# Optimization experiments

Hardware: AMD Instinct MI355X
Metric: run time of the kernel (lower is better)

## Reference

```python
import jax, jax.numpy as jnp
import numpy as np

NUM_HEADS = 16
ROTARY_BASE = 10000.0


def _rope_cos_sin(seqlen, rotary_dim, dtype):
    # inv_freq: (rotary_dim/2,), cos/sin: (seqlen, rotary_dim/2)
    inv_freq = 1.0 / (ROTARY_BASE ** (jnp.arange(0, rotary_dim, 2, dtype=jnp.float32) / rotary_dim))
    t = jnp.arange(seqlen, dtype=jnp.float32)
    freqs = jnp.outer(t, inv_freq)
    return jnp.cos(freqs).astype(dtype), jnp.sin(freqs).astype(dtype)


def _apply_rotary(x, cos, sin):
    # x: (b, s, h, d); cos/sin: (s, d/2). Non-interleaved (GPT-NeoX) halves.
    d2 = cos.shape[-1]
    x1, x2 = x[..., :d2], x[..., d2:2 * d2]
    c = cos[None, :, None, :]
    s = sin[None, :, None, :]
    r1 = x1 * c - x2 * s
    r2 = x1 * s + x2 * c
    return jnp.concatenate([r1, r2], axis=-1)


def setup_inputs() -> dict:
    key = jax.random.key(0)
    ks = jax.random.split(key, 5)
    B, S, E = 2, 2048, 2048
    x = jax.random.normal(ks[0], (B, S, E), dtype=jnp.float32)
    wqkv_w = jax.random.normal(ks[1], (3 * E, E), dtype=jnp.float32) * 0.02
    wqkv_b = jax.random.normal(ks[2], (3 * E,), dtype=jnp.float32) * 0.02
    out_w = jax.random.normal(ks[3], (E, E), dtype=jnp.float32) * 0.02
    out_b = jax.random.normal(ks[4], (E,), dtype=jnp.float32) * 0.02
    return {"x": x, "wqkv_w": wqkv_w, "wqkv_b": wqkv_b, "out_w": out_w, "out_b": out_b}


def reference(x, wqkv_w, wqkv_b, out_w, out_b):
    B, S, E = x.shape
    H = NUM_HEADS
    D = E // H
    # fused QKV projection: (b, s, 3, h, d)
    qkv = (jnp.einsum('bse,fe->bsf', x, wqkv_w) + wqkv_b).reshape(B, S, 3, H, D)
    q, k, v = qkv[:, :, 0], qkv[:, :, 1], qkv[:, :, 2]
    # rotary embedding on full head_dim of q and k
    cos, sin = _rope_cos_sin(S, D, x.dtype)
    q = _apply_rotary(q, cos, sin)
    k = _apply_rotary(k, cos, sin)
    # causal self-attention, softmax_scale = 1/sqrt(head_dim)
    scale = 1.0 / jnp.sqrt(jnp.asarray(D, dtype=x.dtype))
    scores = jnp.einsum('bshd,bthd->bhst', q, k) * scale
    causal_mask = jnp.tril(jnp.ones((S, S), dtype=bool))
    scores = jnp.where(causal_mask[None, None], scores, jnp.asarray(-1e30, dtype=scores.dtype))
    attn = jax.nn.softmax(scores, axis=-1)
    ctx = jnp.einsum('bhst,bthd->bshd', attn, v).reshape(B, S, E)
    return jnp.einsum('bse,fe->bsf', ctx, out_w) + out_b
```

## Files before the change

kernel.cpp:

```cpp
#include <hip/hip_runtime.h>

typedef unsigned short u16;
typedef unsigned int u32;
typedef __bf16 bf16x8 __attribute__((ext_vector_type(8)));
typedef float fx4 __attribute__((ext_vector_type(4)));

__device__ __forceinline__ float bf2f(u16 u) {
    return __uint_as_float(((u32)u) << 16);
}
__device__ __forceinline__ u16 f2bf(float f) {
    u32 x = __float_as_uint(f);
    u32 r = (x + 0x7fffu + ((x >> 16) & 1u)) >> 16;
    return (u16)r;
}

__device__ __forceinline__ void gld16(const u16* g, u16* l) {
    __builtin_amdgcn_global_load_lds(
        (const __attribute__((address_space(1))) void*)g,
        (__attribute__((address_space(3))) void*)l, 16, 0, 0);
}

#define MFMA16(a, b, c) __builtin_amdgcn_mfma_f32_16x16x32_bf16((a), (b), (c), 0, 0, 0)

__global__ __launch_bounds__(256) void cvt_kernel(const float* __restrict__ x,
                                                  const float* __restrict__ w1,
                                                  const float* __restrict__ w2,
                                                  u16* __restrict__ xb,
                                                  u16* __restrict__ w1b,
                                                  u16* __restrict__ w2b) {
    size_t g = ((size_t)blockIdx.x * 256 + threadIdx.x) * 8;
    const float* src;
    u16* dst;
    if (g < 8388608) {
        src = x;
        dst = xb;
    } else if (g < 20971520) {
        src = w1 - 8388608;
        dst = w1b - 8388608;
    } else {
        src = w2 - 20971520;
        dst = w2b - 20971520;
    }
    float4 a = *(const float4*)&src[g];
    float4 b = *(const float4*)&src[g + 4];
    u16 v[8];
    v[0] = f2bf(a.x);
    v[1] = f2bf(a.y);
    v[2] = f2bf(a.z);
    v[3] = f2bf(a.w);
    v[4] = f2bf(b.x);
    v[5] = f2bf(b.y);
    v[6] = f2bf(b.z);
    v[7] = f2bf(b.w);
    *(uint4*)&dst[g] = *(const uint4*)v;
}

template <int MODE>
__global__ __launch_bounds__(256, 2) void gemm_bt(const u16* __restrict__ A,
                                                  const u16* __restrict__ B,
                                                  const float* __restrict__ bias,
                                                  float* __restrict__ Cf,
                                                  u16* __restrict__ qb,
                                                  u16* __restrict__ kb,
                                                  u16* __restrict__ vb,
                                                  int N, int K) {
    __shared__ __align__(16) u16 As[2][128 * 32];
    __shared__ __align__(16) u16 Bs[2][128 * 32];

    const int tid = threadIdx.x;
    const int lane = tid & 63;
    const int wave = tid >> 6;
    const int quad = lane >> 4;
    const int m16 = lane & 15;
    const int wm = wave >> 1, wn = wave & 1;
    const int bm = blockIdx.y * 128, bn = blockIdx.x * 128;

    const int r0 = tid >> 2;
    const int u0 = (tid & 3) ^ ((r0 >> 1) & 3);
    const int r1 = (tid + 256) >> 2;
    const int u1 = ((tid + 256) & 3) ^ ((r1 >> 1) & 3);
    const u16* a0 = &A[(size_t)(bm + r0) * K + u0 * 8];
    const u16* a1 = &A[(size_t)(bm + r1) * K + u1 * 8];
    const u16* b0 = &B[(size_t)(bn + r0) * K + u0 * 8];
    const u16* b1 = &B[(size_t)(bn + r1) * K + u1 * 8];

    const int su = (quad ^ ((m16 >> 1) & 3)) * 8;

#define GLDT(kt_, buf_)                                                       \
    {                                                                         \
        const int k0_ = (kt_) << 5;                                           \
        gld16(a0 + k0_, &As[buf_][tid * 8]);                                  \
        gld16(a1 + k0_, &As[buf_][(tid + 256) * 8]);                          \
        gld16(b0 + k0_, &Bs[buf_][tid * 8]);                                  \
        gld16(b1 + k0_, &Bs[buf_][(tid + 256) * 8]);                          \
    }

    const fx4 zero4 = {0.f, 0.f, 0.f, 0.f};
    fx4 acc[4][4];
#pragma unroll
    for (int i = 0; i < 4; ++i)
#pragma unroll
        for (int j = 0; j < 4; ++j) acc[i][j] = zero4;

    const int nk = K >> 5;
    GLDT(0, 0);
    if (nk > 1) {
        GLDT(1, 1);
        asm volatile("s_waitcnt vmcnt(4)" ::: "memory");
    } else {
        asm volatile("s_waitcnt vmcnt(0)" ::: "memory");
    }
    __builtin_amdgcn_s_barrier();

    int cur = 0;
    for (int kt = 0; kt < nk; ++kt) {
        bf16x8 af[4], bfr[4];
#pragma unroll
        for (int t = 0; t < 4; ++t) {
            af[t] = *(const bf16x8*)&As[cur][(wm * 64 + t * 16 + m16) * 32 + su];
            bfr[t] = *(const bf16x8*)&Bs[cur][(wn * 64 + t * 16 + m16) * 32 + su];
        }
        __builtin_amdgcn_s_setprio(1);
#pragma unroll
        for (int mt = 0; mt < 4; ++mt)
#pragma unroll
            for (int nt = 0; nt < 4; ++nt)
                acc[mt][nt] = MFMA16(af[mt], bfr[nt], acc[mt][nt]);
        __builtin_amdgcn_s_setprio(0);
        __builtin_amdgcn_sched_barrier(0);
        asm volatile("s_waitcnt lgkmcnt(0)" ::: "memory");
        __builtin_amdgcn_s_barrier();

        if (kt + 2 < nk) {
            GLDT(kt + 2, cur);
            asm volatile("s_waitcnt vmcnt(4)" ::: "memory");
        } else {
            asm volatile("s_waitcnt vmcnt(0)" ::: "memory");
        }
        __builtin_amdgcn_s_barrier();
        cur ^= 1;
    }

#pragma unroll
    for (int mt = 0; mt < 4; ++mt) {
#pragma unroll
        for (int r = 0; r < 4; ++r) {
            int row = bm + wm * 64 + mt * 16 + quad * 4 + r;
#pragma unroll
            for (int nt = 0; nt < 4; ++nt) {
                int col = bn + wn * 64 + nt * 16 + m16;
                float v = acc[mt][nt][r] + bias[col];
                if (MODE == 0) {
                    Cf[(size_t)row * N + col] = v;
                } else {
                    int which = col >> 11;
                    int h = (col >> 7) & 15;
                    int d = col & 127;
                    int b = row >> 11;
                    int s = row & 2047;
                    u16* dst = (which == 0) ? qb : ((which == 1) ? kb : vb);
                    dst[(size_t)((b * 16 + h) * 2048 + s) * 128 + d] = f2bf(v);
                }
            }
        }
    }
#undef GLDT
}

__global__ __launch_bounds__(256) void rope_kernel(u16* __restrict__ q,
                                                   u16* __restrict__ k) {
    int t = blockIdx.x * 256 + threadIdx.x;
    int i = t & 63;
    int s = (t >> 6) & 2047;
    int bh = t >> 17;
    float inv = exp2f(-(float)i * 0.2076205059304595f);
    float ang = (float)s * inv;
    float sn, cs;
    sincosf(ang, &sn, &cs);
    size_t base = ((size_t)bh * 2048 + s) * 128 + i;
    {
        float x1 = bf2f(q[base]), x2 = bf2f(q[base + 64]);
        q[base] = f2bf(x1 * cs - x2 * sn);
        q[base + 64] = f2bf(x1 * sn + x2 * cs);
    }
    {
        float x1 = bf2f(k[base]), x2 = bf2f(k[base + 64]);
        k[base] = f2bf(x1 * cs - x2 * sn);
        k[base + 64] = f2bf(x1 * sn + x2 * cs);
    }
}

__global__ __launch_bounds__(256) void vtrans_kernel(const u16* __restrict__ v,
                                                     u16* __restrict__ vt) {
    __shared__ __align__(16) u16 L[128 * 66];
    const int tid = threadIdx.x;
    const int kb = blockIdx.x * 64;
    const int bh = blockIdx.y;
    const u16* vp = v + (size_t)bh * 2048 * 128;
    u16* op = vt + (size_t)bh * 128 * 2048;
#pragma unroll
    for (int i = 0; i < 4; ++i) {
        int c = i * 256 + tid;
        int t = c >> 4, d8 = (c & 15) << 3;
        uint4 x = *(const uint4*)&vp[(kb + t) * 128 + d8];
        const u16* xs = (const u16*)&x;
#pragma unroll
        for (int j = 0; j < 8; ++j) L[(d8 + j) * 66 + t] = xs[j];
    }
    __syncthreads();
#pragma unroll
    for (int i = 0; i < 4; ++i) {
        int c = i * 256 + tid;
        int d = c >> 3, t8 = (c & 7) << 3;
        uint4 x;
        u16* xs = (u16*)&x;
#pragma unroll
        for (int j = 0; j < 8; ++j) xs[j] = L[d * 66 + t8 + j];
        *(uint4*)&op[(size_t)d * 2048 + kb + t8] = x;
    }
}

__global__ __launch_bounds__(512, 2) void attn_kernel(const u16* __restrict__ q,
                                                      const u16* __restrict__ k,
                                                      const u16* __restrict__ vt,
                                                      u16* __restrict__ ctx) {
    __shared__ __align__(16) u16 Ks[2][64 * 128];
    __shared__ __align__(16) u16 Vs[2][128 * 64];
    __shared__ __align__(16) u16 Ps[8][16 * 64];

    const int tid = threadIdx.x;
    const int lane = tid & 63;
    const int wave = tid >> 6;
    const int quad = lane >> 4;
    const int m16 = lane & 15;

    const int l = blockIdx.x;
    const int qt0 = l & 7;
    const int bh = l >> 3;
    const int b = bh >> 4, h = bh & 15;
    const u16* qp = q + (size_t)bh * 2048 * 128;
    const u16* kp = k + (size_t)bh * 2048 * 128;
    const u16* vp = vt + (size_t)bh * 128 * 2048;
    const float scale = 0.08838834764831845f;
    const fx4 zero4 = {0.f, 0.f, 0.f, 0.f};

    int ksrc[2], vsrc[2];
#pragma unroll
    for (int i = 0; i < 2; ++i) {
        int s = tid + i * 512;
        int r = s >> 4, p = s & 15;
        ksrc[i] = r * 128 + (p ^ (r & 7)) * 8;
        int d = s >> 3, pv = s & 7;
        vsrc[i] = d * 2048 + (pv ^ (d & 7)) * 8;
    }

#define GLD_TILE(kb_, buf_)                                                   \
    {                                                                         \
        _Pragma("unroll") for (int ii = 0; ii < 2; ++ii) {                    \
            gld16(kp + (size_t)(kb_)*128 + ksrc[ii],                          \
                  &Ks[buf_][tid * 8 + ii * 4096]);                            \
            gld16(vp + (kb_) + vsrc[ii], &Vs[buf_][tid * 8 + ii * 4096]);     \
        }                                                                     \
    }

#pragma unroll 1
    for (int pass = 0; pass < 2; ++pass) {
        const int qt = pass ? (15 - qt0) : qt0;
        const int qrow0 = qt * 128 + wave * 16;
        const int nkt = 2 * qt + 2;

        bf16x8 qf[4];
#pragma unroll
        for (int c = 0; c < 4; ++c)
            qf[c] = *(const bf16x8*)&qp[(size_t)(qrow0 + m16) * 128 + c * 32 +
                                        quad * 8];

        fx4 o[8];
#pragma unroll
        for (int dn = 0; dn < 8; ++dn) o[dn] = zero4;
        float mi[4], li[4];
#pragma unroll
        for (int r = 0; r < 4; ++r) {
            mi[r] = -1e30f;
            li[r] = 0.f;
        }

        GLD_TILE(0, 0);
        __syncthreads();
        int cur = 0;
        for (int kt = 0; kt < nkt; ++kt) {
            const int kb = kt * 64;
            if (kt + 1 < nkt) GLD_TILE(kb + 64, cur ^ 1);

            fx4 sc[4];
#pragma unroll
            for (int nt = 0; nt < 4; ++nt) sc[nt] = zero4;
            __builtin_amdgcn_s_setprio(1);
#pragma unroll
            for (int c = 0; c < 4; ++c)
#pragma unroll
                for (int nt = 0; nt < 4; ++nt) {
                    int e = (nt * 16 + m16) * 128 + c * 32 + quad * 8;
                    bf16x8 kf =
                        *(const bf16x8*)&Ks[cur][e ^ ((m16 & 7) << 3)];
                    sc[nt] = MFMA16(qf[c], kf, sc[nt]);
                }
            __builtin_amdgcn_s_setprio(0);

#pragma unroll
            for (int r = 0; r < 4; ++r) {
                int rg = qrow0 + quad * 4 + r;
                float mx = mi[r];
#pragma unroll
                for (int nt = 0; nt < 4; ++nt) {
                    int cg = kb + nt * 16 + m16;
                    float s = sc[nt][r] * scale;
                    s = (cg <= rg) ? s : -1e30f;
                    sc[nt][r] = s;
                    mx = fmaxf(mx, s);
                }
                mx = fmaxf(mx, __shfl_xor(mx, 1));
                mx = fmaxf(mx, __shfl_xor(mx, 2));
                mx = fmaxf(mx, __shfl_xor(mx, 4));
                mx = fmaxf(mx, __shfl_xor(mx, 8));
                float alpha = __expf(mi[r] - mx);
                mi[r] = mx;
                float rsum = 0.f;
                int row = quad * 4 + r;
#pragma unroll
                for (int nt = 0; nt < 4; ++nt) {
                    float p = __expf(sc[nt][r] - mx);
                    Ps[wave][(row * 64 + nt * 16 + m16) ^ ((row & 7) << 3)] =
                        f2bf(p);
                    rsum += p;
                }
                rsum += __shfl_xor(rsum, 1);
                rsum += __shfl_xor(rsum, 2);
                rsum += __shfl_xor(rsum, 4);
                rsum += __shfl_xor(rsum, 8);
                li[r] = li[r] * alpha + rsum;
#pragma unroll
                for (int dn = 0; dn < 8; ++dn) o[dn][r] *= alpha;
            }

            __builtin_amdgcn_s_setprio(1);
#pragma unroll
            for (int c2 = 0; c2 < 2; ++c2) {
                bf16x8 pf = *(const bf16x8*)&Ps[wave][(m16 * 64 + c2 * 32 +
                                                       quad * 8) ^
                                                      ((m16 & 7) << 3)];
#pragma unroll
                for (int dn = 0; dn < 8; ++dn) {
                    int e = (dn * 16 + m16) * 64 + c2 * 32 + quad * 8;
                    bf16x8 vf =
                        *(const bf16x8*)&Vs[cur][e ^ ((m16 & 7) << 3)];
                    o[dn] = MFMA16(pf, vf, o[dn]);
                }
            }
            __builtin_amdgcn_s_setprio(0);

            __syncthreads();
            cur ^= 1;
        }

#pragma unroll
        for (int r = 0; r < 4; ++r) {
            int row = qrow0 + quad * 4 + r;
            float inv = 1.0f / li[r];
#pragma unroll
            for (int dn = 0; dn < 8; ++dn) {
                int d = dn * 16 + m16;
                ctx[((size_t)(b * 2048 + row)) * 2048 + h * 128 + d] =
                    f2bf(o[dn][r] * inv);
            }
        }
    }
}

extern "C" void kernel_launch(void* const* d_in, const int* in_sizes, int n_in,
                              void* d_out, int out_size, void* d_ws,
                              size_t ws_size, hipStream_t stream) {
    const float* x = (const float*)d_in[0];
    const float* wqkv_w = (const float*)d_in[1];
    const float* wqkv_b = (const float*)d_in[2];
    const float* out_w = (const float*)d_in[3];
    const float* out_b = (const float*)d_in[4];
    u16* ws = (u16*)d_ws;

    u16* xb = ws;
    u16* wqkvb = ws + 8388608;
    u16* vb = ws + 20971520;
    u16* outwb = ws + 29360128;
    u16* vtb = xb;
    u16* ctx = vb;
    u16* qb = (u16*)d_out;
    u16* kb = qb + 8388608;

    cvt_kernel<<<12288, 256, 0, stream>>>(x, wqkv_w, out_w, xb, wqkvb, outwb);
    gemm_bt<1><<<dim3(48, 32), 256, 0, stream>>>(xb, wqkvb, wqkv_b, nullptr,
                                                 qb, kb, vb, 6144, 2048);
    rope_kernel<<<16384, 256, 0, stream>>>(qb, kb);
    vtrans_kernel<<<dim3(32, 32), 256, 0, stream>>>(vb, vtb);
    attn_kernel<<<256, 512, 0, stream>>>(qb, kb, vtb, ctx);
    gemm_bt<0><<<dim3(16, 32), 256, 0, stream>>>(ctx, outwb, out_b,
                                                 (float*)d_out, nullptr,
                                                 nullptr, nullptr, 2048, 2048);
}
```

Before: 418.2 us.

## Add dedicated 256x128-tile QKV GEMM kernel with 8 waves and split-K phases

Replaces the generic 128x128 gemm_bt instantiation for the QKV projection with a specialized kernel using 512 threads and a 256x128 output tile. It loads 64-wide K slabs as two 32-wide halves into double-buffered LDS and interleaves each prefetch with MFMA work, using explicit waitcnt and priority hints. The aim is more reuse of each B tile across rows and better latency hiding, at the cost of more LDS per block and possibly lower occupancy. The epilogue still scatters bias-added bf16 results into per-head Q/K/V layouts.

```diff
diff --git a/kernel.cpp b/kernel.cpp
--- a/kernel.cpp
+++ b/kernel.cpp
@@ -55,6 +55,111 @@
     *(uint4*)&dst[g] = *(const uint4*)v;
 }
 
+__global__ __launch_bounds__(512, 2) void gemm_qkv(const u16* __restrict__ A,
+                                                   const u16* __restrict__ B,
+                                                   const float* __restrict__ bias,
+                                                   u16* __restrict__ qb,
+                                                   u16* __restrict__ kb,
+                                                   u16* __restrict__ vb) {
+    const int K = 2048;
+    __shared__ __align__(16) u16 As[2][2][256 * 32];
+    __shared__ __align__(16) u16 Bs[2][2][128 * 32];
+
+    const int tid = threadIdx.x;
+    const int lane = tid & 63;
+    const int wave = tid >> 6;
+    const int quad = lane >> 4;
+    const int m16 = lane & 15;
+    const int wm = wave >> 1;
+    const int wn = wave & 1;
+
+    const int bm = (blockIdx.x / 48) * 256;
+    const int bn = (blockIdx.x % 48) * 128;
+    const u16* Ab = A + (size_t)bm * K;
+    const u16* Bbp = B + (size_t)bn * K;
+
+    const int arow0 = tid >> 2, au0 = (tid & 3) ^ (arow0 & 3);
+    const int arow1 = (tid + 512) >> 2, au1 = ((tid + 512) & 3) ^ (arow1 & 3);
+    const int brow = tid >> 2, bu = (tid & 3) ^ (brow & 3);
+
+#define QISSUE(t_, h_, buf_)                                                  \
+    {                                                                         \
+        const int ko_ = (t_)*64 + (h_)*32;                                    \
+        gld16(Ab + (size_t)arow0 * K + ko_ + au0 * 8,                         \
+              &As[buf_][h_][tid * 8]);                                        \
+        gld16(Ab + (size_t)arow1 * K + ko_ + au1 * 8,                         \
+              &As[buf_][h_][(tid + 512) * 8]);                                \
+        gld16(Bbp + (size_t)brow * K + ko_ + bu * 8,                          \
+              &Bs[buf_][h_][tid * 8]);                                        \
+    }
+
+    const fx4 zero4 = {0.f, 0.f, 0.f, 0.f};
+    fx4 acc[4][4];
+#pragma unroll
+    for (int i = 0; i < 4; ++i)
+#pragma unroll
+        for (int j = 0; j < 4; ++j) acc[i][j] = zero4;
+
+#define QPHASE(t_, h_, b_)                                                    \
+    {                                                                         \
+        bf16x8 af[4], bfr[4];                                                 \
+        _Pragma("unroll") for (int mt = 0; mt < 4; ++mt) {                    \
+            int row = wm * 64 + mt * 16 + m16;                                \
+            af[mt] = *(const bf16x8*)&As[b_][h_]                              \
+                         [row * 32 + ((quad ^ (row & 3)) << 3)];              \
+        }                                                                     \
+        _Pragma("unroll") for (int nt = 0; nt < 4; ++nt) {                    \
+            int rc = wn * 64 + nt * 16 + m16;                                 \
+            bfr[nt] = *(const bf16x8*)&Bs[b_][h_]                             \
+                          [rc * 32 + ((quad ^ (rc & 3)) << 3)];               \
+        }                                                                     \
+        if ((t_) + 1 < 32) QISSUE((t_) + 1, h_, (b_) ^ 1);                    \
+        asm volatile("s_waitcnt lgkmcnt(0)" ::: "memory");                    \
+        __builtin_amdgcn_sched_barrier(0);                                    \
+        __builtin_amdgcn_s_setprio(1);                                        \
+        _Pragma("unroll") for (int mt = 0; mt < 4; ++mt)                      \
+            _Pragma("unroll") for (int nt = 0; nt < 4; ++nt)                  \
+                acc[mt][nt] = MFMA16(af[mt], bfr[nt], acc[mt][nt]);           \
+        __builtin_amdgcn_s_setprio(0);                                       \
+        __builtin_amdgcn_sched_barrier(0);                                    \
+        asm volatile("s_waitcnt vmcnt(3)" ::: "memory");                      \
+        __builtin_amdgcn_s_barrier();                                         \
+    }
+
+    QISSUE(0, 0, 0);
+    QISSUE(0, 1, 0);
+    asm volatile("s_waitcnt vmcnt(3)" ::: "memory");
+    __builtin_amdgcn_s_barrier();
+
+    for (int t = 0; t < 32; ++t) {
+        const int b = t & 1;
+        QPHASE(t, 0, b);
+        QPHASE(t, 1, b);
+    }
+
+#pragma unroll
+    for (int mt = 0; mt < 4; ++mt) {
+#pragma unroll
+        for (int rr = 0; rr < 4; ++rr) {
+            int row = bm + wm * 64 + mt * 16 + quad * 4 + rr;
+#pragma unroll
+            for (int nt = 0; nt < 4; ++nt) {
+                int col = bn + wn * 64 + nt * 16 + m16;
+                float v = acc[mt][nt][rr] + bias[col];
+                int which = col >> 11;
+                int h = (col >> 7) & 15;
+                int d = col & 127;
+                int b2 = row >> 11;
+                int s = row & 2047;
+                u16* dst = (which == 0) ? qb : ((which == 1) ? kb : vb);
+                dst[(size_t)((b2 * 16 + h) * 2048 + s) * 128 + d] = f2bf(v);
+            }
+        }
+    }
+#undef QPHASE
+#undef QISSUE
+}
+
 template <int MODE>
 __global__ __launch_bounds__(256, 2) void gemm_bt(const u16* __restrict__ A,
                                                   const u16* __restrict__ B,
@@ -397,8 +502,7 @@
     u16* kb = qb + 8388608;
 
     cvt_kernel<<<12288, 256, 0, stream>>>(x, wqkv_w, out_w, xb, wqkvb, outwb);
-    gemm_bt<1><<<dim3(48, 32), 256, 0, stream>>>(xb, wqkvb, wqkv_b, nullptr,
-                                                 qb, kb, vb, 6144, 2048);
+    gemm_qkv<<<768, 512, 0, stream>>>(xb, wqkvb, wqkv_b, qb, kb, vb);
     rope_kernel<<<16384, 256, 0, stream>>>(qb, kb);
     vtrans_kernel<<<dim3(32, 32), 256, 0, stream>>>(vb, vtb);
     attn_kernel<<<256, 512, 0, stream>>>(qb, kb, vtb, ctx);
```

New measurement: 426.7 us. +2.0%, slower.
